# Optimization experiments

Measured on AMD Instinct MI355X. Metric: run time of the kernel, lower is better.

The kernel has to match this reference:

```python
import jax, jax.numpy as jnp
import numpy as np

N, E, D, H, O = 100000, 1600000, 256, 128, 64


def setup_inputs() -> dict:
    key = jax.random.key(0)
    ks = jax.random.split(key, 10)
    x = jax.random.normal(ks[0], (N, D), dtype=jnp.float32)
    # edges without self loops (original adds remaining self loops itself)
    row = jax.random.randint(ks[1], (E,), 0, N)
    off = jax.random.randint(ks[2], (E,), 1, N)
    col = (row + off) % N
    edge_index = jnp.stack([row, col]).astype(jnp.int64)
    # positive PPMI edge weights (stand-in for cached random-walk PPMI values)
    ppmi_edge_weight = jax.random.uniform(ks[3], (E,), dtype=jnp.float32, minval=0.1, maxval=1.0)
    # glorot-style weights (shared between GCN and PPMI branches, as in the module)
    W1 = jax.random.normal(ks[4], (D, H), dtype=jnp.float32) * np.sqrt(2.0 / (D + H))
    b1 = jnp.zeros((H,), dtype=jnp.float32)
    W2 = jax.random.normal(ks[5], (H, O), dtype=jnp.float32) * np.sqrt(2.0 / (H + O))
    b2 = jnp.zeros((O,), dtype=jnp.float32)
    dense_w = jax.random.normal(ks[6], (O, 1), dtype=jnp.float32) * np.sqrt(2.0 / (O + 1))
    dense_b = jnp.zeros((1,), dtype=jnp.float32)
    return {"x": x, "edge_index": edge_index, "ppmi_edge_weight": ppmi_edge_weight,
            "W1": W1, "b1": b1, "W2": W2, "b2": b2,
            "dense_w": dense_w, "dense_b": dense_b}


def _sym_norm(row, col, ew, n):
    # deg^-0.5[row] * w * deg^-0.5[col], deg from scatter-add over source index
    deg = jax.ops.segment_sum(ew, row, num_segments=n)
    dis = jnp.where(deg > 0, deg ** -0.5, 0.0)
    return dis[row] * ew * dis[col]


def _gconv(h, W, b, row, col, norm, n):
    hw = h @ W                              # [N, F_out]
    msg = norm[:, None] * hw[row]           # gather + scale, [E', F_out]
    return jax.ops.segment_sum(msg, col, num_segments=n) + b


def reference(x, edge_index, ppmi_edge_weight, W1, b1, W2, b2, dense_w, dense_b):
    n = x.shape[0]
    row = edge_index[0].astype(jnp.int32)
    col = edge_index[1].astype(jnp.int32)
    sl = jnp.arange(n, dtype=jnp.int32)
    row_sl = jnp.concatenate([row, sl])
    col_sl = jnp.concatenate([col, sl])
    ones_sl = jnp.ones((n,), dtype=x.dtype)

    # GCN branch: edge_weight = 1, plus self loops (fill_value = 1)
    gcn_ew = jnp.concatenate([jnp.ones((row.shape[0],), dtype=x.dtype), ones_sl])
    gnorm = _sym_norm(row_sl, col_sl, gcn_ew, n)
    g = jax.nn.relu(_gconv(x, W1, b1, row_sl, col_sl, gnorm, n))  # dropout p in eval -> identity
    g = _gconv(g, W2, b2, row_sl, col_sl, gnorm, n)

    # PPMI branch: precomputed positive weights, plus self loops
    ppmi_ew = jnp.concatenate([ppmi_edge_weight.astype(x.dtype), ones_sl])
    pnorm = _sym_norm(row_sl, col_sl, ppmi_ew, n)
    p = jax.nn.relu(_gconv(x, W1, b1, row_sl, col_sl, pnorm, n))
    p = _gconv(p, W2, b2, row_sl, col_sl, pnorm, n)

    stacked = jnp.stack([g, p], axis=1)                 # [N, 2, O]
    logits = stacked @ dense_w + dense_b                # [N, 2, 1]
    w = jax.nn.softmax(logits, axis=1)
    return jnp.sum(stacked * w, axis=1)                 # [N, O]
```

## Files before the change

kernel.cpp:

```cpp
#include <hip/hip_runtime.h>
#include <hip/hip_bf16.h>
#include <math.h>

#define DD 256
#define HH 128
#define OO 64

#define EPB 8192
#define BKT 512

typedef __attribute__((ext_vector_type(8))) __bf16 bf16x8;
typedef __attribute__((ext_vector_type(4))) __bf16 bf16x4;
typedef __attribute__((ext_vector_type(4))) float f32x4;

__device__ inline float2 bf2_to_f2(unsigned u) {
    float2 r;
    r.x = __uint_as_float(u << 16);
    r.y = __uint_as_float(u & 0xffff0000u);
    return r;
}

__global__ void part_count_kernel(const int* __restrict__ row, const int* __restrict__ col,
                                  int e, int nb,
                                  int* __restrict__ cnt_col, int* __restrict__ cnt_row) {
    __shared__ int hc[256], hr[256];
    int t = threadIdx.x;
    hc[t] = 0; hr[t] = 0;
    __syncthreads();
    int base = blockIdx.x * EPB;
    int lim  = min(EPB, e - base);
    for (int i = t; i < lim; i += 256) {
        atomicAdd(&hc[col[base + i] >> 9], 1);
        atomicAdd(&hr[row[base + i] >> 9], 1);
    }
    __syncthreads();
    if (t < nb) {
        cnt_col[blockIdx.x * nb + t] = hc[t];
        cnt_row[blockIdx.x * nb + t] = hr[t];
    }
}

__global__ void scan_blocks_kernel(const int* __restrict__ cnt_col, const int* __restrict__ cnt_row,
                                   int* __restrict__ base_col, int* __restrict__ base_row,
                                   int* __restrict__ tot_col, int* __restrict__ tot_row,
                                   int nblk, int nb) {
    __shared__ int s[256];
    int side = (blockIdx.x >= (unsigned)nb) ? 1 : 0;
    int b = blockIdx.x - side * nb;
    const int* cnt = side ? cnt_row : cnt_col;
    int* base = side ? base_row : base_col;
    int* tot  = side ? tot_row  : tot_col;
    int t = threadIdx.x;
    int v = (t < nblk) ? cnt[(size_t)t * nb + b] : 0;
    s[t] = v;
    __syncthreads();
    for (int off = 1; off < 256; off <<= 1) {
        int u = (t >= off) ? s[t - off] : 0;
        __syncthreads();
        s[t] += u;
        __syncthreads();
    }
    if (t < nblk) base[(size_t)t * nb + b] = s[t] - v;
    if (t == 255) tot[b] = s[255];
}

__global__ void scan_tots_kernel(const int* __restrict__ tot_col, const int* __restrict__ tot_row,
                                 int* __restrict__ bb_col, int* __restrict__ bb_row, int nb) {
    __shared__ int s[256];
    int t = threadIdx.x;
    int v = (t < nb) ? tot_col[t] : 0;
    s[t] = v;
    __syncthreads();
    for (int off = 1; off < 256; off <<= 1) {
        int u = (t >= off) ? s[t - off] : 0;
        __syncthreads();
        s[t] += u;
        __syncthreads();
    }
    if (t < nb) bb_col[t] = s[t] - v;
    __syncthreads();
    int v2 = (t < nb) ? tot_row[t] : 0;
    s[t] = v2;
    __syncthreads();
    for (int off = 1; off < 256; off <<= 1) {
        int u = (t >= off) ? s[t - off] : 0;
        __syncthreads();
        s[t] += u;
        __syncthreads();
    }
    if (t < nb) bb_row[t] = s[t] - v2;
}

__global__ void add_bases_kernel(int* __restrict__ base_col, int* __restrict__ base_row,
                                 const int* __restrict__ bb_col, const int* __restrict__ bb_row,
                                 int* __restrict__ row_ptr, int n, int e, int nblk, int nb) {
    int side = (blockIdx.x >= (unsigned)nb) ? 1 : 0;
    int b = blockIdx.x - side * nb;
    int* base = side ? base_row : base_col;
    int add   = side ? bb_row[b] : bb_col[b];
    for (int t = threadIdx.x; t < nblk; t += blockDim.x) base[(size_t)t * nb + b] += add;
    if (blockIdx.x == 0 && threadIdx.x == 0) row_ptr[n] = e;
}

__global__ void part_scatter_kernel(const int* __restrict__ row, const int* __restrict__ col,
                                    const float* __restrict__ ppmi,
                                    const int* __restrict__ base_col, const int* __restrict__ base_row,
                                    int4* __restrict__ tmp_col, int2* __restrict__ tmp_row,
                                    int e, int nb) {
    __shared__ int cc[256], cr[256];
    int t = threadIdx.x;
    if (t < nb) {
        cc[t] = base_col[blockIdx.x * nb + t];
        cr[t] = base_row[blockIdx.x * nb + t];
    }
    __syncthreads();
    int base = blockIdx.x * EPB;
    int lim  = min(EPB, e - base);
    for (int i = t; i < lim; i += 256) {
        int r = row[base + i], c = col[base + i];
        int w = __float_as_int(ppmi[base + i]);
        int sc = atomicAdd(&cc[c >> 9], 1);
        tmp_col[sc] = make_int4(c, r, w, 0);
        int sr = atomicAdd(&cr[r >> 9], 1);
        tmp_row[sr] = make_int2(r, w);
    }
}

__global__ void deg_bucket_kernel(const int2* __restrict__ tmp_row,
                                  const int* __restrict__ bb_row, const int* __restrict__ tot_row,
                                  float2* __restrict__ dis, int n) {
    __shared__ float dg[BKT], dp[BKT];
    int t = threadIdx.x;
    for (int j = t; j < BKT; j += 256) { dg[j] = 1.0f; dp[j] = 1.0f; }
    __syncthreads();
    int b = blockIdx.x;
    int beg = bb_row[b], cnt = tot_row[b];
    for (int i = t; i < cnt; i += 256) {
        int2 cell = tmp_row[beg + i];
        int lr = cell.x & (BKT - 1);
        atomicAdd(&dg[lr], 1.0f);
        atomicAdd(&dp[lr], __int_as_float(cell.y));
    }
    __syncthreads();
    int rb = b << 9;
    for (int j = t; j < BKT; j += 256) {
        int g = rb + j;
        if (g < n) dis[g] = make_float2(rsqrtf(dg[j]), rsqrtf(dp[j]));
    }
}

__launch_bounds__(512)
__global__ void csr_bucket_kernel(const int4* __restrict__ tmp_col,
                                  const int* __restrict__ bb_col, const int* __restrict__ tot_col,
                                  const float2* __restrict__ dis,
                                  int* __restrict__ row_ptr, int4* __restrict__ csr_meta, int n) {
    __shared__ int hist[BKT], s[BKT], cur[BKT];
    int t = threadIdx.x;
    hist[t] = 0;
    __syncthreads();
    int b = blockIdx.x;
    int beg = bb_col[b], cnt = tot_col[b];
    for (int i = t; i < cnt; i += BKT) atomicAdd(&hist[tmp_col[beg + i].x & (BKT - 1)], 1);
    __syncthreads();
    int own = hist[t];
    s[t] = own;
    __syncthreads();
    for (int off = 1; off < BKT; off <<= 1) {
        int v = (t >= off) ? s[t - off] : 0;
        __syncthreads();
        s[t] += v;
        __syncthreads();
    }
    int gslot = beg + s[t] - own;
    cur[t] = gslot;
    int gc = (b << 9) + t;
    if (gc < n) row_ptr[gc] = gslot;
    __syncthreads();
    for (int i = t; i < cnt; i += BKT) {
        int4 cell = tmp_col[beg + i];
        int lc = cell.x & (BKT - 1);
        int slot = atomicAdd(&cur[lc], 1);
        int r = cell.y;
        float w = __int_as_float(cell.z);
        float2 d = dis[r];
        csr_meta[slot] = make_int4(r, __float_as_int(d.x), __float_as_int(d.y * w), 0);
    }
}

__global__ void conv_w_kernel(const float* __restrict__ W, __bf16* __restrict__ Bh,
                              __bf16* __restrict__ Bl, int K, int N) {
    int i = blockIdx.x * blockDim.x + threadIdx.x;
    if (i >= K * N) return;
    int k = i / N, nn = i % N;
    float v = W[i];
    __bf16 h = (__bf16)v;
    Bh[(size_t)nn * K + k] = h;
    Bl[(size_t)nn * K + k] = (__bf16)(v - (float)h);
}

template<int BM, int BN, typename OT, bool ILV>
__launch_bounds__(256, 2)
__global__ void mfma_gemm_kernel(const float* __restrict__ A,
                                 const __bf16* __restrict__ Bth, const __bf16* __restrict__ Btl,
                                 OT* __restrict__ C, int M, int K, int nHalf) {
    constexpr int BK  = 32;
    constexpr int LDK = BK + 8;
    constexpr int WM  = BM / 4;
    constexpr int MT  = WM / 16;
    constexpr int NT  = BN / 16;
    __shared__ __bf16 Ash[BM * LDK];
    __shared__ __bf16 Asl[BM * LDK];
    __shared__ __bf16 Bsh[BN * LDK];
    __shared__ __bf16 Bsl[BN * LDK];

    const int tid  = threadIdx.x;
    const int wave = tid >> 6;
    const int lane = tid & 63;
    const int quad = lane >> 4;
    const int l16  = lane & 15;
    const int row0 = blockIdx.x * BM;

    f32x4 acc[MT][NT] = {};

    for (int k0 = 0; k0 < K; k0 += BK) {
#pragma unroll
        for (int p = 0; p < BM / 32; ++p) {
            int lin = p * 256 + tid;
            int r   = lin >> 3;
            int kc  = (lin & 7) * 4;
            int gr  = row0 + r;
            float4 v;
            if (gr < M) v = *(const float4*)(A + (size_t)gr * K + k0 + kc);
            else        v = make_float4(0.f, 0.f, 0.f, 0.f);
            __bf16 h0 = (__bf16)v.x, h1 = (__bf16)v.y, h2 = (__bf16)v.z, h3 = (__bf16)v.w;
            __bf16 l0 = (__bf16)(v.x - (float)h0), l1 = (__bf16)(v.y - (float)h1);
            __bf16 l2 = (__bf16)(v.z - (float)h2), l3 = (__bf16)(v.w - (float)h3);
            *(bf16x4*)&Ash[r * LDK + kc] = (bf16x4){h0, h1, h2, h3};
            *(bf16x4*)&Asl[r * LDK + kc] = (bf16x4){l0, l1, l2, l3};
        }
#pragma unroll
        for (int p = 0; p < BN / 64; ++p) {
            int lin = p * 256 + tid;
            int r   = lin >> 2;
            int kc  = (lin & 3) * 8;
            *(uint4*)&Bsh[r * LDK + kc] = *(const uint4*)(Bth + (size_t)r * K + k0 + kc);
            *(uint4*)&Bsl[r * LDK + kc] = *(const uint4*)(Btl + (size_t)r * K + k0 + kc);
        }
        __syncthreads();

        bf16x8 bh[NT], bl[NT];
#pragma unroll
        for (int j = 0; j < NT; ++j) {
            bh[j] = *(const bf16x8*)&Bsh[(j * 16 + l16) * LDK + quad * 8];
            bl[j] = *(const bf16x8*)&Bsl[(j * 16 + l16) * LDK + quad * 8];
        }
#pragma unroll
        for (int i = 0; i < MT; ++i) {
            int m = wave * WM + i * 16 + l16;
            bf16x8 ah = *(const bf16x8*)&Ash[m * LDK + quad * 8];
            bf16x8 al = *(const bf16x8*)&Asl[m * LDK + quad * 8];
#pragma unroll
            for (int j = 0; j < NT; ++j) {
                acc[i][j] = __builtin_amdgcn_mfma_f32_16x16x32_bf16(ah, bh[j], acc[i][j], 0, 0, 0);
                acc[i][j] = __builtin_amdgcn_mfma_f32_16x16x32_bf16(ah, bl[j], acc[i][j], 0, 0, 0);
                acc[i][j] = __builtin_amdgcn_mfma_f32_16x16x32_bf16(al, bh[j], acc[i][j], 0, 0, 0);
            }
        }
        __syncthreads();
    }

#pragma unroll
    for (int i = 0; i < MT; ++i) {
#pragma unroll
        for (int rg = 0; rg < 4; ++rg) {
            int gr = row0 + wave * WM + i * 16 + quad * 4 + rg;
            if (gr < M) {
                if constexpr (ILV) {
                    int s = (gr >= nHalf) ? 1 : 0;
                    size_t base = (size_t)(gr - s * nHalf) * (BN * 2) + s;
#pragma unroll
                    for (int j = 0; j < NT; ++j)
                        C[base + (size_t)(j * 16 + l16) * 2] = (OT)acc[i][j][rg];
                } else {
#pragma unroll
                    for (int j = 0; j < NT; ++j)
                        C[(size_t)gr * BN + j * 16 + l16] = (OT)acc[i][j][rg];
                }
            }
        }
    }
}

__global__ void agg1_pull_kernel(const int* __restrict__ row_ptr, const int4* __restrict__ meta,
                                 const __bf16* __restrict__ hw1,
                                 const float2* __restrict__ dis,
                                 const float* __restrict__ b1,
                                 float* __restrict__ g_out, float* __restrict__ p_out, int n) {
    int c    = blockIdx.x * 4 + (threadIdx.x >> 6);
    int lane = threadIdx.x & 63;
    if (c >= n) return;
    int beg = row_ptr[c], end = row_ptr[c + 1];
    int f2 = lane * 2;
    float sgx = 0.f, sgy = 0.f, spx = 0.f, spy = 0.f;
    int t = beg;
    for (; t + 4 <= end; t += 4) {
        int4 m0 = meta[t], m1 = meta[t + 1], m2 = meta[t + 2], m3 = meta[t + 3];
        unsigned u0 = *(const unsigned*)(hw1 + ((size_t)m0.x << 7) + f2);
        unsigned u1 = *(const unsigned*)(hw1 + ((size_t)m1.x << 7) + f2);
        unsigned u2 = *(const unsigned*)(hw1 + ((size_t)m2.x << 7) + f2);
        unsigned u3 = *(const unsigned*)(hw1 + ((size_t)m3.x << 7) + f2);
        float2 h0 = bf2_to_f2(u0), h1 = bf2_to_f2(u1);
        float2 h2 = bf2_to_f2(u2), h3 = bf2_to_f2(u3);
        float wg0 = __int_as_float(m0.y), wp0 = __int_as_float(m0.z);
        float wg1 = __int_as_float(m1.y), wp1 = __int_as_float(m1.z);
        float wg2 = __int_as_float(m2.y), wp2 = __int_as_float(m2.z);
        float wg3 = __int_as_float(m3.y), wp3 = __int_as_float(m3.z);
        sgx += wg0 * h0.x + wg1 * h1.x + wg2 * h2.x + wg3 * h3.x;
        sgy += wg0 * h0.y + wg1 * h1.y + wg2 * h2.y + wg3 * h3.y;
        spx += wp0 * h0.x + wp1 * h1.x + wp2 * h2.x + wp3 * h3.x;
        spy += wp0 * h0.y + wp1 * h1.y + wp2 * h2.y + wp3 * h3.y;
    }
    for (; t < end; ++t) {
        int4 m0 = meta[t];
        float2 h0 = bf2_to_f2(*(const unsigned*)(hw1 + ((size_t)m0.x << 7) + f2));
        float wg0 = __int_as_float(m0.y), wp0 = __int_as_float(m0.z);
        sgx += wg0 * h0.x; sgy += wg0 * h0.y;
        spx += wp0 * h0.x; spy += wp0 * h0.y;
    }
    float2 d = dis[c];
    size_t idx = ((size_t)c << 7) + f2;
    float2 hs = bf2_to_f2(*(const unsigned*)(hw1 + idx));
    float2 bv = *(const float2*)(b1 + f2);
    float gx = d.x * sgx + d.x * d.x * hs.x + bv.x;
    float gy = d.x * sgy + d.x * d.x * hs.y + bv.y;
    float px = d.y * spx + d.y * d.y * hs.x + bv.x;
    float py = d.y * spy + d.y * d.y * hs.y + bv.y;
    float2 go, po;
    go.x = gx > 0.f ? gx : 0.f;  go.y = gy > 0.f ? gy : 0.f;
    po.x = px > 0.f ? px : 0.f;  po.y = py > 0.f ? py : 0.f;
    *(float2*)&g_out[idx] = go;
    *(float2*)&p_out[idx] = po;
}

__global__ void agg2_final_kernel(const int* __restrict__ row_ptr, const int4* __restrict__ meta,
                                  const __bf16* __restrict__ hw2i,
                                  const float2* __restrict__ dis,
                                  const float* __restrict__ b2,
                                  const float* __restrict__ dense_w, const float* __restrict__ dense_b,
                                  float* __restrict__ out, int n) {
    int c = blockIdx.x * 4 + (threadIdx.x >> 6);
    int f = threadIdx.x & 63;
    if (c >= n) return;
    int beg = row_ptr[c], end = row_ptr[c + 1];
    int f2 = f * 2;
    float sg = 0.f, sp = 0.f;
    int t = beg;
    for (; t + 4 <= end; t += 4) {
        int4 m0 = meta[t], m1 = meta[t + 1], m2 = meta[t + 2], m3 = meta[t + 3];
        unsigned u0 = *(const unsigned*)(hw2i + ((size_t)m0.x << 7) + f2);
        unsigned u1 = *(const unsigned*)(hw2i + ((size_t)m1.x << 7) + f2);
        unsigned u2 = *(const unsigned*)(hw2i + ((size_t)m2.x << 7) + f2);
        unsigned u3 = *(const unsigned*)(hw2i + ((size_t)m3.x << 7) + f2);
        float2 g0 = bf2_to_f2(u0), g1v = bf2_to_f2(u1);
        float2 g2 = bf2_to_f2(u2), g3v = bf2_to_f2(u3);
        sg += __int_as_float(m0.y) * g0.x + __int_as_float(m1.y) * g1v.x
            + __int_as_float(m2.y) * g2.x + __int_as_float(m3.y) * g3v.x;
        sp += __int_as_float(m0.z) * g0.y + __int_as_float(m1.z) * g1v.y
            + __int_as_float(m2.z) * g2.y + __int_as_float(m3.z) * g3v.y;
    }
    for (; t < end; ++t) {
        int4 m0 = meta[t];
        float2 g0 = bf2_to_f2(*(const unsigned*)(hw2i + ((size_t)m0.x << 7) + f2));
        sg += __int_as_float(m0.y) * g0.x;
        sp += __int_as_float(m0.z) * g0.y;
    }
    float2 d = dis[c];
    float2 gps = bf2_to_f2(*(const unsigned*)(hw2i + ((size_t)c << 7) + f2));
    float bb = b2[f];
    float gv = d.x * sg + d.x * d.x * gps.x + bb;
    float pv = d.y * sp + d.y * d.y * gps.y + bb;
    float dwv = dense_w[f];
    float lg = gv * dwv, lp = pv * dwv;
#pragma unroll
    for (int off = 32; off > 0; off >>= 1) {
        lg += __shfl_xor(lg, off, 64);
        lp += __shfl_xor(lp, off, 64);
    }
    lg += dense_b[0];
    lp += dense_b[0];
    float m  = fmaxf(lg, lp);
    float eg = expf(lg - m), ep = expf(lp - m);
    float wgt = eg / (eg + ep);
    out[(size_t)c * OO + f] = wgt * gv + (1.0f - wgt) * pv;
}

extern "C" void kernel_launch(void* const* d_in, const int* in_sizes, int n_in,
                              void* d_out, int out_size, void* d_ws, size_t ws_size,
                              hipStream_t stream) {
    const float* x    = (const float*)d_in[0];
    const int*   ei   = (const int*)d_in[1];
    const float* ppmi = (const float*)d_in[2];
    const float* W1   = (const float*)d_in[3];
    const float* b1   = (const float*)d_in[4];
    const float* W2   = (const float*)d_in[5];
    const float* b2   = (const float*)d_in[6];
    const float* dw   = (const float*)d_in[7];
    const float* db   = (const float*)d_in[8];
    float* out = (float*)d_out;

    const int n = in_sizes[0] / DD;
    const int e = in_sizes[2];
    const int* row = ei;
    const int* col = ei + e;

    const int nb   = (n + BKT - 1) / BKT;
    const int nblk = (e + EPB - 1) / EPB;

    float* ws      = (float*)d_ws;
    float2* dis    = (float2*)ws;
    __bf16* hw1    = (__bf16*)(ws + 2 * (size_t)n);
    float* g1      = (float*)(hw1 + (size_t)n * HH);
    float* p1      = g1 + (size_t)n * HH;
    int4* csr_meta = (int4*)(p1 + (size_t)n * HH);
    __bf16* bt1h   = (__bf16*)(csr_meta + e);
    __bf16* bt1l   = bt1h + (size_t)DD * HH;
    __bf16* bt2h   = bt1l + (size_t)DD * HH;
    __bf16* bt2l   = bt2h + (size_t)HH * OO;
    int* row_ptr   = (int*)(bt2l + (size_t)HH * OO);
    int* cnt_col   = row_ptr + (n + 1);
    int* base_col  = cnt_col + (size_t)nblk * nb;
    int* cnt_row   = base_col + (size_t)nblk * nb;
    int* base_row  = cnt_row + (size_t)nblk * nb;
    int* bb_col    = base_row + (size_t)nblk * nb;
    int* tot_col   = bb_col + nb;
    int* bb_row    = tot_col + nb;
    int* tot_row   = bb_row + nb;
    int4* tmp_col  = (int4*)g1;
    int2* tmp_row  = (int2*)p1;
    __bf16* hw2i   = hw1;

    const int T = 256;

    part_count_kernel<<<nblk, T, 0, stream>>>(row, col, e, nb, cnt_col, cnt_row);
    scan_blocks_kernel<<<2 * nb, T, 0, stream>>>(cnt_col, cnt_row, base_col, base_row,
                                                 tot_col, tot_row, nblk, nb);
    scan_tots_kernel<<<1, T, 0, stream>>>(tot_col, tot_row, bb_col, bb_row, nb);
    add_bases_kernel<<<2 * nb, T, 0, stream>>>(base_col, base_row, bb_col, bb_row,
                                               row_ptr, n, e, nblk, nb);
    part_scatter_kernel<<<nblk, T, 0, stream>>>(row, col, ppmi, base_col, base_row,
                                                tmp_col, tmp_row, e, nb);
    deg_bucket_kernel<<<nb, T, 0, stream>>>(tmp_row, bb_row, tot_row, dis, n);
    csr_bucket_kernel<<<nb, BKT, 0, stream>>>(tmp_col, bb_col, tot_col, dis,
                                              row_ptr, csr_meta, n);

    conv_w_kernel<<<(DD * HH + T - 1) / T, T, 0, stream>>>(W1, bt1h, bt1l, DD, HH);
    conv_w_kernel<<<(HH * OO + T - 1) / T, T, 0, stream>>>(W2, bt2h, bt2l, HH, OO);

    mfma_gemm_kernel<128, HH, __bf16, false><<<(n + 127) / 128, 256, 0, stream>>>(
        x, bt1h, bt1l, hw1, n, DD, 0);
    agg1_pull_kernel<<<(n + 3) / 4, 256, 0, stream>>>(row_ptr, csr_meta, hw1, dis, b1, g1, p1, n);
    mfma_gemm_kernel<128, OO, __bf16, true><<<(2 * n + 127) / 128, 256, 0, stream>>>(
        g1, bt2h, bt2l, hw2i, 2 * n, HH, n);
    agg2_final_kernel<<<(n + 3) / 4, 256, 0, stream>>>(row_ptr, csr_meta, hw2i, dis,
                                                       b2, dw, db, out, n);
}
```

Measured before the change: 554.7 us.

## Fold totals scan into add-bases, widen preprocessing blocks, unroll gathers by eight

Removes the single-block scan_tots launch: each add_bases block now redoes the small totals scan itself and derives its own bucket base. The partition-count, scatter and degree kernels move to 512-thread blocks. Both aggregation kernels' gather loops are unrolled from 4 to 8 edges, with a 4-edge remainder step, so more independent loads are in flight. The costs are redundant scan work per block and higher register pressure in the aggregation loops.

```diff
diff --git a/kernel.cpp b/kernel.cpp
--- a/kernel.cpp
+++ b/kernel.cpp
@@ -25,11 +25,11 @@
                                   int* __restrict__ cnt_col, int* __restrict__ cnt_row) {
     __shared__ int hc[256], hr[256];
     int t = threadIdx.x;
-    hc[t] = 0; hr[t] = 0;
+    if (t < 256) { hc[t] = 0; hr[t] = 0; }
     __syncthreads();
     int base = blockIdx.x * EPB;
     int lim  = min(EPB, e - base);
-    for (int i = t; i < lim; i += 256) {
+    for (int i = t; i < lim; i += 512) {
         atomicAdd(&hc[col[base + i] >> 9], 1);
         atomicAdd(&hr[row[base + i] >> 9], 1);
     }
@@ -64,11 +64,18 @@
     if (t == 255) tot[b] = s[255];
 }
 
-__global__ void scan_tots_kernel(const int* __restrict__ tot_col, const int* __restrict__ tot_row,
-                                 int* __restrict__ bb_col, int* __restrict__ bb_row, int nb) {
+__global__ void add_bases_kernel(int* __restrict__ base_col, int* __restrict__ base_row,
+                                 const int* __restrict__ tot_col, const int* __restrict__ tot_row,
+                                 int* __restrict__ bb_col, int* __restrict__ bb_row,
+                                 int* __restrict__ row_ptr, int n, int e, int nblk, int nb) {
     __shared__ int s[256];
-    int t = threadIdx.x;
-    int v = (t < nb) ? tot_col[t] : 0;
+    __shared__ int bbv;
+    int side = (blockIdx.x >= (unsigned)nb) ? 1 : 0;
+    int b = blockIdx.x - side * nb;
+    const int* tot = side ? tot_row : tot_col;
+    int* base = side ? base_row : base_col;
+    int t = threadIdx.x;
+    int v = (t < nb) ? tot[t] : 0;
     s[t] = v;
     __syncthreads();
     for (int off = 1; off < 256; off <<= 1) {
@@ -77,29 +84,14 @@
         s[t] += u;
         __syncthreads();
     }
-    if (t < nb) bb_col[t] = s[t] - v;
-    __syncthreads();
-    int v2 = (t < nb) ? tot_row[t] : 0;
-    s[t] = v2;
-    __syncthreads();
-    for (int off = 1; off < 256; off <<= 1) {
-        int u = (t >= off) ? s[t - off] : 0;
-        __syncthreads();
-        s[t] += u;
-        __syncthreads();
-    }
-    if (t < nb) bb_row[t] = s[t] - v2;
-}
-
-__global__ void add_bases_kernel(int* __restrict__ base_col, int* __restrict__ base_row,
-                                 const int* __restrict__ bb_col, const int* __restrict__ bb_row,
-                                 int* __restrict__ row_ptr, int n, int e, int nblk, int nb) {
-    int side = (blockIdx.x >= (unsigned)nb) ? 1 : 0;
-    int b = blockIdx.x - side * nb;
-    int* base = side ? base_row : base_col;
-    int add   = side ? bb_row[b] : bb_col[b];
-    for (int t = threadIdx.x; t < nblk; t += blockDim.x) base[(size_t)t * nb + b] += add;
-    if (blockIdx.x == 0 && threadIdx.x == 0) row_ptr[n] = e;
+    if (t == 0) {
+        bbv = (b > 0) ? s[b - 1] : 0;
+        (side ? bb_row : bb_col)[b] = bbv;
+    }
+    __syncthreads();
+    int add = bbv;
+    for (int j = t; j < nblk; j += blockDim.x) base[(size_t)j * nb + b] += add;
+    if (blockIdx.x == 0 && t == 0) row_ptr[n] = e;
 }
 
 __global__ void part_scatter_kernel(const int* __restrict__ row, const int* __restrict__ col,
@@ -116,7 +108,7 @@
     __syncthreads();
     int base = blockIdx.x * EPB;
     int lim  = min(EPB, e - base);
-    for (int i = t; i < lim; i += 256) {
+    for (int i = t; i < lim; i += 512) {
         int r = row[base + i], c = col[base + i];
         int w = __float_as_int(ppmi[base + i]);
         int sc = atomicAdd(&cc[c >> 9], 1);
@@ -131,22 +123,19 @@
                                   float2* __restrict__ dis, int n) {
     __shared__ float dg[BKT], dp[BKT];
     int t = threadIdx.x;
-    for (int j = t; j < BKT; j += 256) { dg[j] = 1.0f; dp[j] = 1.0f; }
+    dg[t] = 1.0f; dp[t] = 1.0f;
     __syncthreads();
     int b = blockIdx.x;
     int beg = bb_row[b], cnt = tot_row[b];
-    for (int i = t; i < cnt; i += 256) {
+    for (int i = t; i < cnt; i += 512) {
         int2 cell = tmp_row[beg + i];
         int lr = cell.x & (BKT - 1);
         atomicAdd(&dg[lr], 1.0f);
         atomicAdd(&dp[lr], __int_as_float(cell.y));
     }
     __syncthreads();
-    int rb = b << 9;
-    for (int j = t; j < BKT; j += 256) {
-        int g = rb + j;
-        if (g < n) dis[g] = make_float2(rsqrtf(dg[j]), rsqrtf(dp[j]));
-    }
+    int g = (b << 9) + t;
+    if (g < n) dis[g] = make_float2(rsqrtf(dg[t]), rsqrtf(dp[t]));
 }
 
 __launch_bounds__(512)
@@ -303,22 +292,38 @@
     int f2 = lane * 2;
     float sgx = 0.f, sgy = 0.f, spx = 0.f, spy = 0.f;
     int t = beg;
-    for (; t + 4 <= end; t += 4) {
-        int4 m0 = meta[t], m1 = meta[t + 1], m2 = meta[t + 2], m3 = meta[t + 3];
-        unsigned u0 = *(const unsigned*)(hw1 + ((size_t)m0.x << 7) + f2);
-        unsigned u1 = *(const unsigned*)(hw1 + ((size_t)m1.x << 7) + f2);
-        unsigned u2 = *(const unsigned*)(hw1 + ((size_t)m2.x << 7) + f2);
-        unsigned u3 = *(const unsigned*)(hw1 + ((size_t)m3.x << 7) + f2);
-        float2 h0 = bf2_to_f2(u0), h1 = bf2_to_f2(u1);
-        float2 h2 = bf2_to_f2(u2), h3 = bf2_to_f2(u3);
-        float wg0 = __int_as_float(m0.y), wp0 = __int_as_float(m0.z);
-        float wg1 = __int_as_float(m1.y), wp1 = __int_as_float(m1.z);
-        float wg2 = __int_as_float(m2.y), wp2 = __int_as_float(m2.z);
-        float wg3 = __int_as_float(m3.y), wp3 = __int_as_float(m3.z);
-        sgx += wg0 * h0.x + wg1 * h1.x + wg2 * h2.x + wg3 * h3.x;
-        sgy += wg0 * h0.y + wg1 * h1.y + wg2 * h2.y + wg3 * h3.y;
-        spx += wp0 * h0.x + wp1 * h1.x + wp2 * h2.x + wp3 * h3.x;
-        spy += wp0 * h0.y + wp1 * h1.y + wp2 * h2.y + wp3 * h3.y;
+    for (; t + 8 <= end; t += 8) {
+        int4 m[8];
+#pragma unroll
+        for (int q = 0; q < 8; ++q) m[q] = meta[t + q];
+        unsigned u[8];
+#pragma unroll
+        for (int q = 0; q < 8; ++q)
+            u[q] = *(const unsigned*)(hw1 + ((size_t)m[q].x << 7) + f2);
+#pragma unroll
+        for (int q = 0; q < 8; ++q) {
+            float2 h = bf2_to_f2(u[q]);
+            float wg = __int_as_float(m[q].y), wp = __int_as_float(m[q].z);
+            sgx += wg * h.x; sgy += wg * h.y;
+            spx += wp * h.x; spy += wp * h.y;
+        }
+    }
+    if (t + 4 <= end) {
+        int4 m[4];
+#pragma unroll
+        for (int q = 0; q < 4; ++q) m[q] = meta[t + q];
+        unsigned u[4];
+#pragma unroll
+        for (int q = 0; q < 4; ++q)
+            u[q] = *(const unsigned*)(hw1 + ((size_t)m[q].x << 7) + f2);
+#pragma unroll
+        for (int q = 0; q < 4; ++q) {
+            float2 h = bf2_to_f2(u[q]);
+            float wg = __int_as_float(m[q].y), wp = __int_as_float(m[q].z);
+            sgx += wg * h.x; sgy += wg * h.y;
+            spx += wp * h.x; spy += wp * h.y;
+        }
+        t += 4;
     }
     for (; t < end; ++t) {
         int4 m0 = meta[t];
@@ -355,18 +360,36 @@
     int f2 = f * 2;
     float sg = 0.f, sp = 0.f;
     int t = beg;
-    for (; t + 4 <= end; t += 4) {
-        int4 m0 = meta[t], m1 = meta[t + 1], m2 = meta[t + 2], m3 = meta[t + 3];
-        unsigned u0 = *(const unsigned*)(hw2i + ((size_t)m0.x << 7) + f2);
-        unsigned u1 = *(const unsigned*)(hw2i + ((size_t)m1.x << 7) + f2);
-        unsigned u2 = *(const unsigned*)(hw2i + ((size_t)m2.x << 7) + f2);
-        unsigned u3 = *(const unsigned*)(hw2i + ((size_t)m3.x << 7) + f2);
-        float2 g0 = bf2_to_f2(u0), g1v = bf2_to_f2(u1);
-        float2 g2 = bf2_to_f2(u2), g3v = bf2_to_f2(u3);
-        sg += __int_as_float(m0.y) * g0.x + __int_as_float(m1.y) * g1v.x
-            + __int_as_float(m2.y) * g2.x + __int_as_float(m3.y) * g3v.x;
-        sp += __int_as_float(m0.z) * g0.y + __int_as_float(m1.z) * g1v.y
-            + __int_as_float(m2.z) * g2.y + __int_as_float(m3.z) * g3v.y;
+    for (; t + 8 <= end; t += 8) {
+        int4 m[8];
+#pragma unroll
+        for (int q = 0; q < 8; ++q) m[q] = meta[t + q];
+        unsigned u[8];
+#pragma unroll
+        for (int q = 0; q < 8; ++q)
+            u[q] = *(const unsigned*)(hw2i + ((size_t)m[q].x << 7) + f2);
+#pragma unroll
+        for (int q = 0; q < 8; ++q) {
+            float2 g0 = bf2_to_f2(u[q]);
+            sg += __int_as_float(m[q].y) * g0.x;
+            sp += __int_as_float(m[q].z) * g0.y;
+        }
+    }
+    if (t + 4 <= end) {
+        int4 m[4];
+#pragma unroll
+        for (int q = 0; q < 4; ++q) m[q] = meta[t + q];
+        unsigned u[4];
+#pragma unroll
+        for (int q = 0; q < 4; ++q)
+            u[q] = *(const unsigned*)(hw2i + ((size_t)m[q].x << 7) + f2);
+#pragma unroll
+        for (int q = 0; q < 4; ++q) {
+            float2 g0 = bf2_to_f2(u[q]);
+            sg += __int_as_float(m[q].y) * g0.x;
+            sp += __int_as_float(m[q].z) * g0.y;
+        }
+        t += 4;
     }
     for (; t < end; ++t) {
         int4 m0 = meta[t];
@@ -441,15 +464,14 @@
 
     const int T = 256;
 
-    part_count_kernel<<<nblk, T, 0, stream>>>(row, col, e, nb, cnt_col, cnt_row);
+    part_count_kernel<<<nblk, 512, 0, stream>>>(row, col, e, nb, cnt_col, cnt_row);
     scan_blocks_kernel<<<2 * nb, T, 0, stream>>>(cnt_col, cnt_row, base_col, base_row,
                                                  tot_col, tot_row, nblk, nb);
-    scan_tots_kernel<<<1, T, 0, stream>>>(tot_col, tot_row, bb_col, bb_row, nb);
-    add_bases_kernel<<<2 * nb, T, 0, stream>>>(base_col, base_row, bb_col, bb_row,
-                                               row_ptr, n, e, nblk, nb);
-    part_scatter_kernel<<<nblk, T, 0, stream>>>(row, col, ppmi, base_col, base_row,
-                                                tmp_col, tmp_row, e, nb);
-    deg_bucket_kernel<<<nb, T, 0, stream>>>(tmp_row, bb_row, tot_row, dis, n);
+    add_bases_kernel<<<2 * nb, T, 0, stream>>>(base_col, base_row, tot_col, tot_row,
+                                               bb_col, bb_row, row_ptr, n, e, nblk, nb);
+    part_scatter_kernel<<<nblk, 512, 0, stream>>>(row, col, ppmi, base_col, base_row,
+                                                  tmp_col, tmp_row, e, nb);
+    deg_bucket_kernel<<<nb, 512, 0, stream>>>(tmp_row, bb_row, tot_row, dis, n);
     csr_bucket_kernel<<<nb, BKT, 0, stream>>>(tmp_col, bb_col, tot_col, dis,
                                               row_ptr, csr_meta, n);
 
```

Result: faster. 524.8 us (-5.4%).
